# Kernel optimization log

Measured on AMD Instinct MI355X. Metric: run time of the kernel, lower is better.

Reference implementation:

```python
import jax, jax.numpy as jnp
import numpy as np
import math

D_MODEL = 1024
NUM_HEADS = 16
BATCH = 2
SEQ = 2048

def setup_inputs() -> dict:
    key = jax.random.key(0)
    ks = jax.random.split(key, 9)
    s = 1.0 / math.sqrt(D_MODEL)
    inp = {
        "X": jax.random.normal(ks[0], (BATCH, SEQ, D_MODEL), dtype=jnp.float32),
        "Wq": jax.random.uniform(ks[1], (D_MODEL, D_MODEL), jnp.float32, -s, s),
        "bq": jax.random.uniform(ks[2], (D_MODEL,), jnp.float32, -s, s),
        "Wk": jax.random.uniform(ks[3], (D_MODEL, D_MODEL), jnp.float32, -s, s),
        "bk": jax.random.uniform(ks[4], (D_MODEL,), jnp.float32, -s, s),
        "Wv": jax.random.uniform(ks[5], (D_MODEL, D_MODEL), jnp.float32, -s, s),
        "bv": jax.random.uniform(ks[6], (D_MODEL,), jnp.float32, -s, s),
        "Wo": jax.random.uniform(ks[7], (D_MODEL, D_MODEL), jnp.float32, -s, s),
        "bo": jax.random.uniform(ks[8], (D_MODEL,), jnp.float32, -s, s),
    }
    return inp

def reference(X, Wq, bq, Wk, bk, Wv, bv, Wo, bo):
    B, S, D = X.shape
    H = NUM_HEADS
    dk = D // H
    # QKV projections (Linear: x @ W.T + b; here W stored as [in, out] so x @ W + b)
    q = X @ Wq + bq
    k = X @ Wk + bk
    v = X @ Wv + bv
    # split heads -> [B, H, S, dk]
    q = q.reshape(B, S, H, dk).transpose(0, 2, 1, 3)
    k = k.reshape(B, S, H, dk).transpose(0, 2, 1, 3)
    v = v.reshape(B, S, H, dk).transpose(0, 2, 1, 3)
    scores = jnp.einsum("bhqd,bhkd->bhqk", q, k) / math.sqrt(dk)
    weights = jax.nn.softmax(scores, axis=-1)
    attn = jnp.einsum("bhqk,bhkd->bhqd", weights, v)
    concat = attn.transpose(0, 2, 1, 3).reshape(B, S, D)
    return concat @ Wo + bo
```

## Files before the change

kernel.cpp:

```cpp
#include <hip/hip_runtime.h>
#include <stdint.h>

#define D_MODEL 1024
#define NH      16
#define DKH     64
#define BATCH   2
#define SEQ     2048
#define M_TOK   (BATCH*SEQ)

typedef __attribute__((ext_vector_type(8))) short bf16x8;
typedef __attribute__((ext_vector_type(4))) float f32x4;

__device__ __forceinline__ uint16_t f2b(float f) {
  uint32_t u = __builtin_bit_cast(uint32_t, f);
  return (uint16_t)((u + 0x7FFFu + ((u >> 16) & 1u)) >> 16);
}

__device__ __forceinline__ void gl2lds16(const uint16_t* g, uint16_t* l) {
  __builtin_amdgcn_global_load_lds(
      (const __attribute__((address_space(1))) void*)g,
      (__attribute__((address_space(3))) void*)l, 16, 0, 0);
}

__global__ void convx(const float* __restrict__ X, uint16_t* __restrict__ Xb) {
  int i = (blockIdx.x * 256 + threadIdx.x) * 8;
  float4 a = *(const float4*)(X + i);
  float4 b = *(const float4*)(X + i + 4);
  uint16_t tmp[8] = {f2b(a.x), f2b(a.y), f2b(a.z), f2b(a.w),
                     f2b(b.x), f2b(b.y), f2b(b.z), f2b(b.w)};
  *(uint4*)(Xb + i) = *(const uint4*)tmp;
}

__global__ void wtrans(const float* __restrict__ W0, const float* __restrict__ W1,
                       const float* __restrict__ W2, const float* __restrict__ W3,
                       uint16_t* __restrict__ T0, uint16_t* __restrict__ T1,
                       uint16_t* __restrict__ T2, uint16_t* __restrict__ T3) {
  __shared__ float tile[32][33];
  int z = blockIdx.z;
  const float* W = (z == 0) ? W0 : (z == 1) ? W1 : (z == 2) ? W2 : W3;
  uint16_t*    T = (z == 0) ? T0 : (z == 1) ? T1 : (z == 2) ? T2 : T3;
  int k0 = blockIdx.x * 32, n0 = blockIdx.y * 32;
  int tx = threadIdx.x, ty = threadIdx.y;
  tile[ty][tx] = W[(size_t)(k0 + ty) * D_MODEL + n0 + tx];
  __syncthreads();
  T[(size_t)(n0 + ty) * D_MODEL + k0 + tx] = f2b(tile[tx][ty]);
}

template <bool SWAP>
__device__ __forceinline__ void gemm_core(const uint16_t* __restrict__ A,
                                          const uint16_t* __restrict__ BT,
                                          uint16_t* As, uint16_t* Bs,
                                          int m0, int n0, int kBeg, int kEnd,
                                          f32x4 (&acc)[4][4]) {
  const int t    = threadIdx.x;
  const int lane = t & 63;
  const int qi   = lane & 15, g = lane >> 4;
  const int wm   = (t >> 7) & 1;
  const int wn   = (t >> 6) & 1;
  const int srow = t >> 2;
  const int sc   = (t & 3) ^ ((t >> 3) & 3);
  const int wbase = t & 192;
  const int rch  = (g ^ ((qi >> 1) & 3)) * 8;

  const uint16_t* Ag = A  + (size_t)(m0 + srow) * D_MODEL + sc * 8;
  const uint16_t* Bg = BT + (size_t)(n0 + srow) * D_MODEL + sc * 8;

#pragma unroll
  for (int j = 0; j < 2; j++) {
    gl2lds16(Ag + (size_t)j * 64 * D_MODEL + kBeg, As + (j * 256 + wbase) * 8);
    gl2lds16(Bg + (size_t)j * 64 * D_MODEL + kBeg, Bs + (j * 256 + wbase) * 8);
  }

  int cur = 0;
  for (int k0 = kBeg; k0 < kEnd; k0 += 32) {
    __syncthreads();
    int kn = k0 + 32;
    if (kn < kEnd) {
      int nb = (cur ^ 1) * 4096;
#pragma unroll
      for (int j = 0; j < 2; j++) {
        gl2lds16(Ag + (size_t)j * 64 * D_MODEL + kn, As + nb + (j * 256 + wbase) * 8);
        gl2lds16(Bg + (size_t)j * 64 * D_MODEL + kn, Bs + nb + (j * 256 + wbase) * 8);
      }
    }
    const uint16_t* Ab = As + cur * 4096;
    const uint16_t* Bb = Bs + cur * 4096;
    bf16x8 af[4], bf[4];
#pragma unroll
    for (int i = 0; i < 4; i++) {
      af[i] = *(const bf16x8*)(Ab + (wm * 64 + i * 16 + qi) * 32 + rch);
      bf[i] = *(const bf16x8*)(Bb + (wn * 64 + i * 16 + qi) * 32 + rch);
    }
#pragma unroll
    for (int i = 0; i < 4; i++)
#pragma unroll
      for (int j = 0; j < 4; j++)
        acc[i][j] = SWAP
          ? __builtin_amdgcn_mfma_f32_16x16x32_bf16(bf[j], af[i], acc[i][j], 0, 0, 0)
          : __builtin_amdgcn_mfma_f32_16x16x32_bf16(af[i], bf[j], acc[i][j], 0, 0, 0);
    cur ^= 1;
  }
}

__global__ __launch_bounds__(256) void qkv_gemm(
    const uint16_t* __restrict__ Xb,
    const uint16_t* __restrict__ WqT, const uint16_t* __restrict__ WkT,
    const uint16_t* __restrict__ WvT,
    const float* __restrict__ bq, const float* __restrict__ bk,
    const float* __restrict__ bv,
    uint16_t* __restrict__ Qo, uint16_t* __restrict__ Ko, uint16_t* __restrict__ Vt) {
  __shared__ __align__(16) uint16_t smem[17408];
  uint16_t* As = smem;
  uint16_t* Bs = smem + 8192;
  uint16_t* T  = smem;
  const int z = blockIdx.z;
  const uint16_t* BT  = (z == 0) ? WqT : (z == 1) ? WkT : WvT;
  const float*   bias = (z == 0) ? bq  : (z == 1) ? bk  : bv;
  const int m0 = blockIdx.x * 128, n0 = blockIdx.y * 128;
  const int lane = threadIdx.x & 63, qi = lane & 15, g = lane >> 4;
  const int wm = (threadIdx.x >> 7) & 1, wn = (threadIdx.x >> 6) & 1;
  const float l2e = 1.4426950408889634f * 0.125f;

  const f32x4 ZERO = {0.f, 0.f, 0.f, 0.f};
  f32x4 acc[4][4];
#pragma unroll
  for (int i = 0; i < 4; i++)
#pragma unroll
    for (int j = 0; j < 4; j++) acc[i][j] = ZERO;

  if (z == 2) {
    gemm_core<false>(Xb, BT, As, Bs, m0, n0, 0, D_MODEL, acc);
    __syncthreads();
#pragma unroll
    for (int i = 0; i < 4; i++) {
      int tok = wm * 64 + i * 16 + g * 4;
#pragma unroll
      for (int j = 0; j < 4; j++) {
        int ch = wn * 64 + j * 16 + qi;
        float bb = bias[n0 + ch];
        uint32_t lo = (uint32_t)f2b(acc[i][j][0] + bb) | ((uint32_t)f2b(acc[i][j][1] + bb) << 16);
        uint32_t hi = (uint32_t)f2b(acc[i][j][2] + bb) | ((uint32_t)f2b(acc[i][j][3] + bb) << 16);
        uint2 pk = {lo, hi};
        *(uint2*)(T + ch * 136 + tok) = pk;
      }
    }
    __syncthreads();
    {
      int ch = threadIdx.x >> 1, sh = threadIdx.x & 1;
      const uint16_t* src = T + ch * 136 + sh * 64;
      int bidx = m0 >> 11;
      uint16_t* dst = Vt + ((size_t)(bidx * D_MODEL + n0 + ch)) * SEQ + (m0 & 2047) + sh * 64;
#pragma unroll
      for (int u = 0; u < 8; u++)
        *(uint4*)(dst + u * 8) = *(const uint4*)(src + u * 8);
    }
  } else {
    gemm_core<true>(Xb, BT, As, Bs, m0, n0, 0, D_MODEL, acc);
    uint16_t* O = z ? Ko : Qo;
    const float osc = (z == 0) ? l2e : 1.0f;
#pragma unroll
    for (int i = 0; i < 4; i++) {
      size_t tok = m0 + wm * 64 + i * 16 + qi;
#pragma unroll
      for (int j = 0; j < 4; j++) {
        int ch = n0 + wn * 64 + j * 16 + g * 4;
        float4 bb = *(const float4*)(bias + ch);
        uint32_t lo = (uint32_t)f2b((acc[i][j][0] + bb.x) * osc) |
                      ((uint32_t)f2b((acc[i][j][1] + bb.y) * osc) << 16);
        uint32_t hi = (uint32_t)f2b((acc[i][j][2] + bb.z) * osc) |
                      ((uint32_t)f2b((acc[i][j][3] + bb.w) * osc) << 16);
        uint2 pk = {lo, hi};
        *(uint2*)(O + tok * D_MODEL + ch) = pk;
      }
    }
  }
}

__global__ __launch_bounds__(256) void oproj_gemm(
    const uint16_t* __restrict__ Ab, const uint16_t* __restrict__ WoT,
    const float* __restrict__ bo, float* __restrict__ out) {
  __shared__ __align__(16) uint16_t As[8192];
  __shared__ __align__(16) uint16_t Bs[8192];
  const int m0 = blockIdx.x * 128, n0 = blockIdx.y * 128;
  const f32x4 ZERO = {0.f, 0.f, 0.f, 0.f};
  f32x4 acc[4][4];
#pragma unroll
  for (int i = 0; i < 4; i++)
#pragma unroll
    for (int j = 0; j < 4; j++) acc[i][j] = ZERO;

  gemm_core<true>(Ab, WoT, As, Bs, m0, n0, 0, D_MODEL, acc);

  const int lane = threadIdx.x & 63, qi = lane & 15, g = lane >> 4;
  const int wm = (threadIdx.x >> 7) & 1, wn = (threadIdx.x >> 6) & 1;
#pragma unroll
  for (int i = 0; i < 4; i++) {
    size_t tok = m0 + wm * 64 + i * 16 + qi;
#pragma unroll
    for (int j = 0; j < 4; j++) {
      int ch = n0 + wn * 64 + j * 16 + g * 4;
      float4 bb = *(const float4*)(bo + ch);
      float4 o = {acc[i][j][0] + bb.x, acc[i][j][1] + bb.y,
                  acc[i][j][2] + bb.z, acc[i][j][3] + bb.w};
      *(float4*)(out + tok * D_MODEL + ch) = o;
    }
  }
}

__global__ __launch_bounds__(256) void attn_fwd(
    const uint16_t* __restrict__ Q, const uint16_t* __restrict__ K,
    const uint16_t* __restrict__ Vt, uint16_t* __restrict__ O) {
  __shared__ __align__(16) uint16_t sm[25600];
  uint16_t* Q0 = sm;
  uint16_t* Q1 = sm + 4096;
  uint16_t* K0 = sm + 8192;
  uint16_t* K1 = sm + 10240;
  uint16_t* V0 = sm + 12288;
  uint16_t* V1 = sm + 14336;
  uint16_t* Ps = sm + 16384;

  const int t = threadIdx.x, lane = t & 63, w = t >> 6;
  const int g = lane >> 4, qi = lane & 15;
  const int wbase = t & 192;
  const int sc = (t & 3) ^ ((t >> 3) & 3);
  const int rch = (g ^ ((qi >> 1) & 3)) * 8;
  const int q0 = blockIdx.x * 128;
  const int bh = blockIdx.y, b = bh >> 4, h = bh & 15;
  const uint16_t* Qp = Q + (size_t)b * SEQ * D_MODEL + h * DKH;
  const uint16_t* Kp = K + (size_t)b * SEQ * D_MODEL + h * DKH;
  const uint16_t* Vp = Vt + (size_t)bh * DKH * SEQ;

#pragma unroll
  for (int hs = 0; hs < 2; hs++) {
    uint16_t* Qs = hs ? Q1 : Q0;
#pragma unroll
    for (int j = 0; j < 2; j++) {
      int row = j * 64 + (t >> 2);
      gl2lds16(Qp + (size_t)(q0 + row) * D_MODEL + hs * 32 + sc * 8,
               Qs + (j * 256 + wbase) * 8);
    }
  }

  float lsum[2] = {0.f, 0.f};
  const f32x4 ZERO = {0.f, 0.f, 0.f, 0.f};
  f32x4 oaccT[4][2];
#pragma unroll
  for (int d = 0; d < 4; d++)
#pragma unroll
    for (int i = 0; i < 2; i++) oaccT[d][i] = ZERO;

  for (int kt = 0; kt < SEQ / 64; kt++) {
    __syncthreads();
    {
      int row = t >> 2, c8 = sc * 8;
      const uint16_t* Kr = Kp + (size_t)(kt * 64 + row) * D_MODEL;
      const uint16_t* Vr = Vp + (size_t)row * SEQ + kt * 64;
      gl2lds16(Kr + c8,       K0 + wbase * 8);
      gl2lds16(Kr + 32 + c8,  K1 + wbase * 8);
      gl2lds16(Vr + c8,       V0 + wbase * 8);
      gl2lds16(Vr + 32 + c8,  V1 + wbase * 8);
    }
    __syncthreads();

    f32x4 sacc[4][2];
#pragma unroll
    for (int j = 0; j < 4; j++)
#pragma unroll
      for (int i = 0; i < 2; i++) sacc[j][i] = ZERO;
#pragma unroll
    for (int ks = 0; ks < 2; ks++) {
      const uint16_t* Ksb = ks ? K1 : K0;
      const uint16_t* Qsb = ks ? Q1 : Q0;
      bf16x8 kf[4], qf[2];
#pragma unroll
      for (int j = 0; j < 4; j++)
        kf[j] = *(const bf16x8*)(Ksb + (j * 16 + qi) * 32 + rch);
#pragma unroll
      for (int i = 0; i < 2; i++)
        qf[i] = *(const bf16x8*)(Qsb + (w * 32 + i * 16 + qi) * 32 + rch);
#pragma unroll
      for (int j = 0; j < 4; j++)
#pragma unroll
        for (int i = 0; i < 2; i++)
          sacc[j][i] = __builtin_amdgcn_mfma_f32_16x16x32_bf16(kf[j], qf[i], sacc[j][i], 0, 0, 0);
    }

#pragma unroll
    for (int i = 0; i < 2; i++) {
      uint16_t* Pr = Ps + (w * 32 + i * 16 + qi) * 72;
#pragma unroll
      for (int j = 0; j < 4; j++) {
        float p0 = __builtin_amdgcn_exp2f(sacc[j][i][0]);
        float p1 = __builtin_amdgcn_exp2f(sacc[j][i][1]);
        float p2 = __builtin_amdgcn_exp2f(sacc[j][i][2]);
        float p3 = __builtin_amdgcn_exp2f(sacc[j][i][3]);
        lsum[i] += (p0 + p1) + (p2 + p3);
        uint2 pk = {__builtin_amdgcn_perm(__builtin_bit_cast(uint32_t, p1),
                                          __builtin_bit_cast(uint32_t, p0), 0x07060302u),
                    __builtin_amdgcn_perm(__builtin_bit_cast(uint32_t, p3),
                                          __builtin_bit_cast(uint32_t, p2), 0x07060302u)};
        *(uint2*)(Pr + j * 16 + g * 4) = pk;
      }
    }
    __syncthreads();

#pragma unroll
    for (int ks = 0; ks < 2; ks++) {
      const uint16_t* Vsb = ks ? V1 : V0;
      bf16x8 vf[4], pf[2];
#pragma unroll
      for (int d = 0; d < 4; d++)
        vf[d] = *(const bf16x8*)(Vsb + (d * 16 + qi) * 32 + rch);
#pragma unroll
      for (int i = 0; i < 2; i++)
        pf[i] = *(const bf16x8*)(Ps + (w * 32 + i * 16 + qi) * 72 + ks * 32 + g * 8);
#pragma unroll
      for (int d = 0; d < 4; d++)
#pragma unroll
        for (int i = 0; i < 2; i++)
          oaccT[d][i] = __builtin_amdgcn_mfma_f32_16x16x32_bf16(vf[d], pf[i], oaccT[d][i], 0, 0, 0);
    }
  }

#pragma unroll
  for (int i = 0; i < 2; i++) {
    lsum[i] += __shfl_xor(lsum[i], 16, 64);
    lsum[i] += __shfl_xor(lsum[i], 32, 64);
  }
  float rl[2] = {1.f / lsum[0], 1.f / lsum[1]};

#pragma unroll
  for (int i = 0; i < 2; i++) {
    size_t row = (size_t)b * SEQ + q0 + w * 32 + i * 16 + qi;
#pragma unroll
    for (int d = 0; d < 4; d++) {
      uint32_t lo = (uint32_t)f2b(oaccT[d][i][0] * rl[i]) |
                    ((uint32_t)f2b(oaccT[d][i][1] * rl[i]) << 16);
      uint32_t hi = (uint32_t)f2b(oaccT[d][i][2] * rl[i]) |
                    ((uint32_t)f2b(oaccT[d][i][3] * rl[i]) << 16);
      uint2 pk = {lo, hi};
      *(uint2*)(O + row * D_MODEL + h * DKH + d * 16 + g * 4) = pk;
    }
  }
}

extern "C" void kernel_launch(void* const* d_in, const int* in_sizes, int n_in,
                              void* d_out, int out_size, void* d_ws, size_t ws_size,
                              hipStream_t stream) {
  (void)in_sizes; (void)n_in; (void)out_size; (void)ws_size;
  const float* X  = (const float*)d_in[0];
  const float* Wq = (const float*)d_in[1];
  const float* bq = (const float*)d_in[2];
  const float* Wk = (const float*)d_in[3];
  const float* bk = (const float*)d_in[4];
  const float* Wv = (const float*)d_in[5];
  const float* bv = (const float*)d_in[6];
  const float* Wo = (const float*)d_in[7];
  const float* bo = (const float*)d_in[8];
  float* out = (float*)d_out;

  char* p = (char*)d_ws;
  uint16_t* Xb  = (uint16_t*)p; p += (size_t)M_TOK * D_MODEL * 2;
  uint16_t* WqT = (uint16_t*)p; p += (size_t)D_MODEL * D_MODEL * 2;
  uint16_t* WkT = (uint16_t*)p; p += (size_t)D_MODEL * D_MODEL * 2;
  uint16_t* WvT = (uint16_t*)p; p += (size_t)D_MODEL * D_MODEL * 2;
  uint16_t* WoT = (uint16_t*)p; p += (size_t)D_MODEL * D_MODEL * 2;
  uint16_t* Qw  = (uint16_t*)p; p += (size_t)M_TOK * D_MODEL * 2;
  uint16_t* Kw  = (uint16_t*)p; p += (size_t)M_TOK * D_MODEL * 2;
  uint16_t* Vt  = (uint16_t*)p; p += (size_t)M_TOK * D_MODEL * 2;
  uint16_t* Ob  = (uint16_t*)p; p += (size_t)M_TOK * D_MODEL * 2;

  convx<<<(M_TOK * D_MODEL) / (256 * 8), 256, 0, stream>>>(X, Xb);
  wtrans<<<dim3(32, 32, 4), dim3(32, 32), 0, stream>>>(Wq, Wk, Wv, Wo, WqT, WkT, WvT, WoT);
  qkv_gemm<<<dim3(32, 8, 3), 256, 0, stream>>>(Xb, WqT, WkT, WvT, bq, bk, bv, Qw, Kw, Vt);
  attn_fwd<<<dim3(SEQ / 128, BATCH * NH), 256, 0, stream>>>(Qw, Kw, Vt, Ob);
  oproj_gemm<<<dim3(32, 8), 256, 0, stream>>>(Ob, WoT, bo, out);
}
```

Before: 208.3 us.

## Double-buffer K/V in attention, hoist Q fragments, retile O-projection to 128x64

The attention kernel now prefetches the next K/V tile into a second LDS buffer while computing the current one. It cuts the per-iteration barriers from three to one, relying on each wave reading only its own P rows. Q MFMA fragments are loaded into registers once instead of every key tile. The output-projection GEMM gets its own double-buffered loop with a 128x64 tile and twice as many blocks, for better CU fill, at the cost of more LDS in attention and more repeated A loads in the GEMM.

```diff
diff --git a/kernel.cpp b/kernel.cpp
--- a/kernel.cpp
+++ b/kernel.cpp
@@ -180,25 +180,64 @@
     const uint16_t* __restrict__ Ab, const uint16_t* __restrict__ WoT,
     const float* __restrict__ bo, float* __restrict__ out) {
   __shared__ __align__(16) uint16_t As[8192];
-  __shared__ __align__(16) uint16_t Bs[8192];
-  const int m0 = blockIdx.x * 128, n0 = blockIdx.y * 128;
+  __shared__ __align__(16) uint16_t Bs[4096];
+  const int t = threadIdx.x;
+  const int lane = t & 63, qi = lane & 15, g = lane >> 4;
+  const int wm = (t >> 7) & 1;
+  const int wn = (t >> 6) & 1;
+  const int srow = t >> 2;
+  const int sc = (t & 3) ^ ((t >> 3) & 3);
+  const int wbase = t & 192;
+  const int rch = (g ^ ((qi >> 1) & 3)) * 8;
+  const int m0 = blockIdx.x * 128, n0 = blockIdx.y * 64;
+
+  const uint16_t* Ag = Ab  + (size_t)(m0 + srow) * D_MODEL + sc * 8;
+  const uint16_t* Bg = WoT + (size_t)(n0 + srow) * D_MODEL + sc * 8;
+
   const f32x4 ZERO = {0.f, 0.f, 0.f, 0.f};
-  f32x4 acc[4][4];
+  f32x4 acc[4][2];
 #pragma unroll
   for (int i = 0; i < 4; i++)
 #pragma unroll
-    for (int j = 0; j < 4; j++) acc[i][j] = ZERO;
-
-  gemm_core<true>(Ab, WoT, As, Bs, m0, n0, 0, D_MODEL, acc);
-
-  const int lane = threadIdx.x & 63, qi = lane & 15, g = lane >> 4;
-  const int wm = (threadIdx.x >> 7) & 1, wn = (threadIdx.x >> 6) & 1;
+    for (int j = 0; j < 2; j++) acc[i][j] = ZERO;
+
+  gl2lds16(Ag, As + wbase * 8);
+  gl2lds16(Ag + (size_t)64 * D_MODEL, As + (256 + wbase) * 8);
+  gl2lds16(Bg, Bs + wbase * 8);
+
+  int cur = 0;
+  for (int k0 = 0; k0 < D_MODEL; k0 += 32) {
+    __syncthreads();
+    int kn = k0 + 32;
+    if (kn < D_MODEL) {
+      int nbA = (cur ^ 1) * 4096, nbB = (cur ^ 1) * 2048;
+      gl2lds16(Ag + kn, As + nbA + wbase * 8);
+      gl2lds16(Ag + (size_t)64 * D_MODEL + kn, As + nbA + (256 + wbase) * 8);
+      gl2lds16(Bg + kn, Bs + nbB + wbase * 8);
+    }
+    const uint16_t* Abuf = As + cur * 4096;
+    const uint16_t* Bbuf = Bs + cur * 2048;
+    bf16x8 af[4], bf[2];
+#pragma unroll
+    for (int i = 0; i < 4; i++)
+      af[i] = *(const bf16x8*)(Abuf + (wm * 64 + i * 16 + qi) * 32 + rch);
+#pragma unroll
+    for (int j = 0; j < 2; j++)
+      bf[j] = *(const bf16x8*)(Bbuf + (wn * 32 + j * 16 + qi) * 32 + rch);
+#pragma unroll
+    for (int i = 0; i < 4; i++)
+#pragma unroll
+      for (int j = 0; j < 2; j++)
+        acc[i][j] = __builtin_amdgcn_mfma_f32_16x16x32_bf16(bf[j], af[i], acc[i][j], 0, 0, 0);
+    cur ^= 1;
+  }
+
 #pragma unroll
   for (int i = 0; i < 4; i++) {
     size_t tok = m0 + wm * 64 + i * 16 + qi;
 #pragma unroll
-    for (int j = 0; j < 4; j++) {
-      int ch = n0 + wn * 64 + j * 16 + g * 4;
+    for (int j = 0; j < 2; j++) {
+      int ch = n0 + wn * 32 + j * 16 + g * 4;
       float4 bb = *(const float4*)(bo + ch);
       float4 o = {acc[i][j][0] + bb.x, acc[i][j][1] + bb.y,
                   acc[i][j][2] + bb.z, acc[i][j][3] + bb.w};
@@ -210,14 +249,8 @@
 __global__ __launch_bounds__(256) void attn_fwd(
     const uint16_t* __restrict__ Q, const uint16_t* __restrict__ K,
     const uint16_t* __restrict__ Vt, uint16_t* __restrict__ O) {
-  __shared__ __align__(16) uint16_t sm[25600];
-  uint16_t* Q0 = sm;
-  uint16_t* Q1 = sm + 4096;
-  uint16_t* K0 = sm + 8192;
-  uint16_t* K1 = sm + 10240;
-  uint16_t* V0 = sm + 12288;
-  uint16_t* V1 = sm + 14336;
-  uint16_t* Ps = sm + 16384;
+  __shared__ __align__(16) uint16_t sm[33792];
+  uint16_t* Ps = sm + 24576;
 
   const int t = threadIdx.x, lane = t & 63, w = t >> 6;
   const int g = lane >> 4, qi = lane & 15;
@@ -230,16 +263,30 @@
   const uint16_t* Kp = K + (size_t)b * SEQ * D_MODEL + h * DKH;
   const uint16_t* Vp = Vt + (size_t)bh * DKH * SEQ;
 
-#pragma unroll
-  for (int hs = 0; hs < 2; hs++) {
-    uint16_t* Qs = hs ? Q1 : Q0;
-#pragma unroll
-    for (int j = 0; j < 2; j++) {
-      int row = j * 64 + (t >> 2);
-      gl2lds16(Qp + (size_t)(q0 + row) * D_MODEL + hs * 32 + sc * 8,
-               Qs + (j * 256 + wbase) * 8);
-    }
-  }
+  const int srow = t >> 2, c8 = sc * 8;
+
+#pragma unroll
+  for (int hs = 0; hs < 2; hs++)
+#pragma unroll
+    for (int j = 0; j < 2; j++)
+      gl2lds16(Qp + (size_t)(q0 + j * 64 + srow) * D_MODEL + hs * 32 + c8,
+               sm + hs * 4096 + (j * 256 + wbase) * 8);
+  {
+    const uint16_t* Kr = Kp + (size_t)srow * D_MODEL;
+    const uint16_t* Vr = Vp + (size_t)srow * SEQ;
+    gl2lds16(Kr + c8,      sm + 8192 + wbase * 8);
+    gl2lds16(Kr + 32 + c8, sm + 8192 + 2048 + wbase * 8);
+    gl2lds16(Vr + c8,      sm + 16384 + wbase * 8);
+    gl2lds16(Vr + 32 + c8, sm + 16384 + 2048 + wbase * 8);
+  }
+  __syncthreads();
+
+  bf16x8 qf[2][2];
+#pragma unroll
+  for (int ks = 0; ks < 2; ks++)
+#pragma unroll
+    for (int i = 0; i < 2; i++)
+      qf[ks][i] = *(const bf16x8*)(sm + ks * 4096 + (w * 32 + i * 16 + qi) * 32 + rch);
 
   float lsum[2] = {0.f, 0.f};
   const f32x4 ZERO = {0.f, 0.f, 0.f, 0.f};
@@ -249,18 +296,19 @@
 #pragma unroll
     for (int i = 0; i < 2; i++) oaccT[d][i] = ZERO;
 
+  int cur = 0;
   for (int kt = 0; kt < SEQ / 64; kt++) {
-    __syncthreads();
-    {
-      int row = t >> 2, c8 = sc * 8;
-      const uint16_t* Kr = Kp + (size_t)(kt * 64 + row) * D_MODEL;
-      const uint16_t* Vr = Vp + (size_t)row * SEQ + kt * 64;
-      gl2lds16(Kr + c8,       K0 + wbase * 8);
-      gl2lds16(Kr + 32 + c8,  K1 + wbase * 8);
-      gl2lds16(Vr + c8,       V0 + wbase * 8);
-      gl2lds16(Vr + 32 + c8,  V1 + wbase * 8);
-    }
-    __syncthreads();
+    if (kt + 1 < SEQ / 64) {
+      int nb = (cur ^ 1) * 4096;
+      const uint16_t* Kr = Kp + (size_t)((kt + 1) * 64 + srow) * D_MODEL;
+      const uint16_t* Vr = Vp + (size_t)srow * SEQ + (kt + 1) * 64;
+      gl2lds16(Kr + c8,      sm + 8192 + nb + wbase * 8);
+      gl2lds16(Kr + 32 + c8, sm + 8192 + nb + 2048 + wbase * 8);
+      gl2lds16(Vr + c8,      sm + 16384 + nb + wbase * 8);
+      gl2lds16(Vr + 32 + c8, sm + 16384 + nb + 2048 + wbase * 8);
+    }
+    const uint16_t* Kb = sm + 8192 + cur * 4096;
+    const uint16_t* Vb = sm + 16384 + cur * 4096;
 
     f32x4 sacc[4][2];
 #pragma unroll
@@ -269,20 +317,16 @@
       for (int i = 0; i < 2; i++) sacc[j][i] = ZERO;
 #pragma unroll
     for (int ks = 0; ks < 2; ks++) {
-      const uint16_t* Ksb = ks ? K1 : K0;
-      const uint16_t* Qsb = ks ? Q1 : Q0;
-      bf16x8 kf[4], qf[2];
+      const uint16_t* Ksb = Kb + ks * 2048;
+      bf16x8 kf[4];
 #pragma unroll
       for (int j = 0; j < 4; j++)
         kf[j] = *(const bf16x8*)(Ksb + (j * 16 + qi) * 32 + rch);
 #pragma unroll
-      for (int i = 0; i < 2; i++)
-        qf[i] = *(const bf16x8*)(Qsb + (w * 32 + i * 16 + qi) * 32 + rch);
-#pragma unroll
       for (int j = 0; j < 4; j++)
 #pragma unroll
         for (int i = 0; i < 2; i++)
-          sacc[j][i] = __builtin_amdgcn_mfma_f32_16x16x32_bf16(kf[j], qf[i], sacc[j][i], 0, 0, 0);
+          sacc[j][i] = __builtin_amdgcn_mfma_f32_16x16x32_bf16(kf[j], qf[ks][i], sacc[j][i], 0, 0, 0);
     }
 
 #pragma unroll
@@ -302,11 +346,10 @@
         *(uint2*)(Pr + j * 16 + g * 4) = pk;
       }
     }
-    __syncthreads();
 
 #pragma unroll
     for (int ks = 0; ks < 2; ks++) {
-      const uint16_t* Vsb = ks ? V1 : V0;
+      const uint16_t* Vsb = Vb + ks * 2048;
       bf16x8 vf[4], pf[2];
 #pragma unroll
       for (int d = 0; d < 4; d++)
@@ -320,6 +363,9 @@
         for (int i = 0; i < 2; i++)
           oaccT[d][i] = __builtin_amdgcn_mfma_f32_16x16x32_bf16(vf[d], pf[i], oaccT[d][i], 0, 0, 0);
     }
+
+    if (kt + 1 < SEQ / 64) __syncthreads();
+    cur ^= 1;
   }
 
 #pragma unroll
@@ -374,5 +420,5 @@
   wtrans<<<dim3(32, 32, 4), dim3(32, 32), 0, stream>>>(Wq, Wk, Wv, Wo, WqT, WkT, WvT, WoT);
   qkv_gemm<<<dim3(32, 8, 3), 256, 0, stream>>>(Xb, WqT, WkT, WvT, bq, bk, bv, Qw, Kw, Vt);
   attn_fwd<<<dim3(SEQ / 128, BATCH * NH), 256, 0, stream>>>(Qw, Kw, Vt, Ob);
-  oproj_gemm<<<dim3(32, 8), 256, 0, stream>>>(Ob, WoT, bo, out);
-}
+  oproj_gemm<<<dim3(32, 16), 256, 0, stream>>>(Ob, WoT, bo, out);
+}
```

New measurement: 204.2 us. 2.0% less time.
